# Kernel tuning notes

Hardware: AMD Instinct MI355X
Metric: run time of the kernel (lower is better)

## Reference

```python
import jax, jax.numpy as jnp
import numpy as np

B, N, M, C, H = 256, 4096, 64, 512, 4
IN, OUT = 64, 64
EPS = 1e-8

def setup_inputs():
    key = jax.random.key(0)
    ks = jax.random.split(key, 8)
    def w(k, shape, scale=0.05):
        return jax.random.normal(k, shape, dtype=jnp.float32) * scale
    return {
        "in_data": jax.random.normal(ks[0], (B, IN), dtype=jnp.float32),
        "memory": jax.random.normal(ks[1], (B, N, M), dtype=jnp.float32),
        "h0": jnp.zeros((B, C), jnp.float32),
        "c0": jnp.zeros((B, C), jnp.float32),
        "prev_weights": jnp.zeros((2 * H, B, N), jnp.float32),
        "prev_reads": jax.random.normal(ks[2], (H, B, M), dtype=jnp.float32),
        "W_ih": w(ks[3], (4 * C, IN + H * M)),
        "b_ih": jnp.zeros((4 * C,), jnp.float32),
        "W_hh": w(ks[4], (4 * C, C)),
        "b_hh": jnp.zeros((4 * C,), jnp.float32),
        "W_out": w(ks[5], (OUT, C + H * M)),
        "b_out": jnp.zeros((OUT,), jnp.float32),
        "W_addr": w(ks[6], (2 * H, M + 6, C)),
        "b_addr": jnp.zeros((2 * H, M + 6), jnp.float32),
        "W_ea": w(ks[7], (H, 2 * M, C)),
        "b_ea": jnp.zeros((H, 2 * M), jnp.float32),
    }


def reference(in_data, memory, h0, c0, prev_weights, prev_reads,
              W_ih, b_ih, W_hh, b_hh, W_out, b_out,
              W_addr, b_addr, W_ea, b_ea):
    # ---- controller: LSTMCell over [input, prev_reads...] ----
    x = jnp.concatenate([in_data] + [prev_reads[i] for i in range(H)], axis=-1)  # [B, IN+H*M]
    gates = x @ W_ih.T + b_ih + h0 @ W_hh.T + b_hh                               # [B, 4C]
    i_g, f_g, g_g, o_g = jnp.split(gates, 4, axis=-1)
    c = jax.nn.sigmoid(f_g) * c0 + jax.nn.sigmoid(i_g) * jnp.tanh(g_g)
    h = jax.nn.sigmoid(o_g) * jnp.tanh(c)

    # ---- heads: alternate read / write, sequential over memory ----
    mem = memory
    reads = []
    for hi in range(2 * H):
        p = c @ W_addr[hi].T + b_addr[hi]                     # [B, M+6]
        k = jnp.tanh(p[:, :M])                                # key
        beta = jax.nn.softplus(p[:, M:M + 1])                 # key strength
        gate = jax.nn.sigmoid(p[:, M + 1:M + 2])              # interpolation gate
        s = jax.nn.softmax(p[:, M + 2:M + 5], axis=-1)        # shift weights (3)
        gamma = 1.0 + jax.nn.softplus(p[:, M + 5:M + 6])      # sharpening
        # content addressing: cosine similarity against all memory rows
        dot = jnp.einsum('bnm,bm->bn', mem, k)                # [B, N]
        norms = jnp.linalg.norm(mem, axis=-1) * jnp.linalg.norm(k, axis=-1, keepdims=True)
        wc = jax.nn.softmax(beta * dot / (norms + EPS), axis=-1)
        # interpolation with previous weights
        wg = gate * wc + (1.0 - gate) * prev_weights[hi]
        # circular shift convolution (shifts -1, 0, +1)
        ws = (s[:, 0:1] * jnp.roll(wg, 1, axis=-1)
              + s[:, 1:2] * wg
              + s[:, 2:3] * jnp.roll(wg, -1, axis=-1))
        # sharpening
        wp = ws ** gamma
        w = wp / (jnp.sum(wp, axis=-1, keepdims=True) + EPS)
        if hi % 2 == 0:  # read head
            reads.append(jnp.einsum('bn,bnm->bm', w, mem))
        else:            # write head: erase then add
            ea = c @ W_ea[hi // 2].T + b_ea[hi // 2]          # [B, 2M]
            e = jax.nn.sigmoid(ea[:, :M])
            a = jnp.tanh(ea[:, M:])
            mem = mem * (1.0 - w[:, :, None] * e[:, None, :]) + w[:, :, None] * a[:, None, :]

    # ---- output layer over [h, reads...] ----
    state = jnp.concatenate([h] + reads, axis=-1)             # [B, C+H*M]
    return jax.nn.sigmoid(state @ W_out.T + b_out)            # [B, OUT]
```

## Files before the change

kernel.cpp:

```cpp
#include <hip/hip_runtime.h>
#include <hip/hip_fp16.h>
#include <math.h>

#define EPSF 1e-8f
#define NN 4096
#define BB 256
#define PH ((size_t)BB * NN)

__device__ __forceinline__ float sigf(float x) { return 1.0f / (1.0f + expf(-x)); }
__device__ __forceinline__ float softplusf(float x) { return x > 20.0f ? x : log1pf(expf(x)); }
__device__ __forceinline__ float dot4(float4 a, float4 b) {
  return a.x * b.x + a.y * b.y + a.z * b.z + a.w * b.w;
}
__device__ __forceinline__ unsigned short f2bf(float x) {
  unsigned int u = __float_as_uint(x);
  unsigned int r = (u + 0x7FFF + ((u >> 16) & 1)) >> 16;
  return (unsigned short)r;
}
__device__ __forceinline__ float bf2f(unsigned int lo16) {
  return __uint_as_float(lo16 << 16);
}

__device__ __forceinline__ float gather_x(const float* __restrict__ in_data,
                                          const float* __restrict__ prev_reads,
                                          const float* __restrict__ h0,
                                          int row, int k) {
  if (k < 64) return in_data[row * 64 + k];
  if (k < 320) { int i = (k - 64) >> 6, m = (k - 64) & 63; return prev_reads[((size_t)i * 256 + row) * 64 + m]; }
  return h0[row * 512 + (k - 320)];
}

__global__ __launch_bounds__(256) void gemm_gates_kernel(
    const float* __restrict__ in_data, const float* __restrict__ prev_reads,
    const float* __restrict__ h0, const float* __restrict__ W_ih,
    const float* __restrict__ W_hh, const float* __restrict__ b_ih,
    const float* __restrict__ b_hh, float* __restrict__ gates) {
  __shared__ float As[16][33];
  __shared__ float Ws[16][65];
  int tid = threadIdx.x, tx = tid & 15, ty = tid >> 4;
  int row0 = blockIdx.y * 32, col0 = blockIdx.x * 64;
  float acc[2][4] = {{0,0,0,0},{0,0,0,0}};
  for (int k0 = 0; k0 < 832; k0 += 16) {
    const float* Wp; int kw, KW;
    if (k0 < 320) { Wp = W_ih; kw = k0; KW = 320; }
    else          { Wp = W_hh; kw = k0 - 320; KW = 512; }
    for (int i = tid; i < 32 * 16; i += 256) {
      int rr = i >> 4, cc = i & 15;
      As[cc][rr] = gather_x(in_data, prev_reads, h0, row0 + rr, k0 + cc);
    }
    for (int i = tid; i < 64 * 16; i += 256) {
      int rr = i >> 4, cc = i & 15;
      Ws[cc][rr] = Wp[(size_t)(col0 + rr) * KW + kw + cc];
    }
    __syncthreads();
#pragma unroll
    for (int kk = 0; kk < 16; kk++) {
      float a0 = As[kk][ty * 2 + 0], a1 = As[kk][ty * 2 + 1];
      float w0 = Ws[kk][tx * 4 + 0], w1 = Ws[kk][tx * 4 + 1];
      float w2 = Ws[kk][tx * 4 + 2], w3 = Ws[kk][tx * 4 + 3];
      acc[0][0] += a0 * w0; acc[0][1] += a0 * w1; acc[0][2] += a0 * w2; acc[0][3] += a0 * w3;
      acc[1][0] += a1 * w0; acc[1][1] += a1 * w1; acc[1][2] += a1 * w2; acc[1][3] += a1 * w3;
    }
    __syncthreads();
  }
  for (int i = 0; i < 2; i++)
    for (int j = 0; j < 4; j++) {
      int cc = col0 + tx * 4 + j;
      gates[(size_t)(row0 + ty * 2 + i) * 2048 + cc] = acc[i][j] + b_ih[cc] + b_hh[cc];
    }
}

__global__ void lstm_elem_kernel(const float* __restrict__ gates,
                                 const float* __restrict__ c0,
                                 float* __restrict__ c, float* __restrict__ h) {
  int idx = blockIdx.x * 256 + threadIdx.x;
  if (idx >= 256 * 512) return;
  int b = idx >> 9, u = idx & 511;
  const float* g = gates + (size_t)b * 2048;
  float ig = sigf(g[u]), fg = sigf(g[512 + u]);
  float gg = tanhf(g[1024 + u]), og = sigf(g[1536 + u]);
  float cv = fg * c0[idx] + ig * gg;
  c[idx] = cv;
  h[idx] = og * tanhf(cv);
}

__global__ __launch_bounds__(256) void gemm_heads_kernel(
    const float* __restrict__ C, const float* __restrict__ W_addr,
    const float* __restrict__ W_ea, const float* __restrict__ b_addr,
    const float* __restrict__ b_ea, float* __restrict__ p_raw) {
  __shared__ float As[16][33];
  __shared__ float Ws[16][65];
  int tid = threadIdx.x, tx = tid & 15, ty = tid >> 4;
  int row0 = blockIdx.y * 32, col0 = blockIdx.x * 64;
  float acc[2][4] = {{0,0,0,0},{0,0,0,0}};
  for (int k0 = 0; k0 < 512; k0 += 16) {
    for (int i = tid; i < 32 * 16; i += 256) {
      int rr = i >> 4, cc = i & 15;
      As[cc][rr] = C[(size_t)(row0 + rr) * 512 + k0 + cc];
    }
    for (int i = tid; i < 64 * 16; i += 256) {
      int rr = i >> 4, cc = i & 15;
      int col = col0 + rr;
      float v = 0.f;
      if (col < 560) v = W_addr[(size_t)col * 512 + k0 + cc];
      else if (col < 1072) v = W_ea[(size_t)(col - 560) * 512 + k0 + cc];
      Ws[cc][rr] = v;
    }
    __syncthreads();
#pragma unroll
    for (int kk = 0; kk < 16; kk++) {
      float a0 = As[kk][ty * 2 + 0], a1 = As[kk][ty * 2 + 1];
      float w0 = Ws[kk][tx * 4 + 0], w1 = Ws[kk][tx * 4 + 1];
      float w2 = Ws[kk][tx * 4 + 2], w3 = Ws[kk][tx * 4 + 3];
      acc[0][0] += a0 * w0; acc[0][1] += a0 * w1; acc[0][2] += a0 * w2; acc[0][3] += a0 * w3;
      acc[1][0] += a1 * w0; acc[1][1] += a1 * w1; acc[1][2] += a1 * w2; acc[1][3] += a1 * w3;
    }
    __syncthreads();
  }
  for (int i = 0; i < 2; i++)
    for (int j = 0; j < 4; j++) {
      int col = col0 + tx * 4 + j;
      if (col < 1072) {
        float bias = col < 560 ? b_addr[col] : b_ea[col - 560];
        p_raw[(size_t)(row0 + ty * 2 + i) * 1072 + col] = acc[i][j] + bias;
      }
    }
}

__global__ void params_kernel(const float* __restrict__ p_raw,
    float* __restrict__ knorm, float* __restrict__ betav,
    float* __restrict__ gatev, float* __restrict__ sv,
    float* __restrict__ gammav, float* __restrict__ combo,
    float* __restrict__ scal) {
  int b = blockIdx.x, m = threadIdx.x;
  const float* p = p_raw + (size_t)b * 1072;
  float kv[7];
#pragma unroll
  for (int hi = 0; hi < 7; hi++) {
    float k = tanhf(p[hi * 70 + m]);
    kv[hi] = k;
    float s = k * k;
#pragma unroll
    for (int d = 1; d < 64; d <<= 1) s += __shfl_xor(s, d);
    if (m == 0) {
      int hb = hi * BB + b;
      knorm[hb] = sqrtf(s);
      betav[hb] = softplusf(p[hi * 70 + 64]);
      gatev[hb] = sigf(p[hi * 70 + 65]);
      float a0 = p[hi * 70 + 66], a1 = p[hi * 70 + 67], a2 = p[hi * 70 + 68];
      float mm = fmaxf(a0, fmaxf(a1, a2));
      float e0 = expf(a0 - mm), e1 = expf(a1 - mm), e2 = expf(a2 - mm);
      float es = e0 + e1 + e2;
      sv[hb * 3 + 0] = e0 / es; sv[hb * 3 + 1] = e1 / es; sv[hb * 3 + 2] = e2 / es;
      gammav[hb] = 1.0f + softplusf(p[hi * 70 + 69]);
    }
  }
  float e1 = sigf(p[560 + 0 * 128 + m]),  a1v = tanhf(p[560 + 0 * 128 + 64 + m]);
  float e3 = sigf(p[560 + 1 * 128 + m]),  a3v = tanhf(p[560 + 1 * 128 + 64 + m]);
  float e5 = sigf(p[560 + 2 * 128 + m]),  a5v = tanhf(p[560 + 2 * 128 + 64 + m]);
  size_t bm = (size_t)b * 64 + m;
  combo[0 * 16384 + bm] = kv[0];  combo[1 * 16384 + bm] = kv[1];
  combo[2 * 16384 + bm] = kv[2];  combo[3 * 16384 + bm] = e1 * kv[2];
  combo[4 * 16384 + bm] = kv[3];  combo[5 * 16384 + bm] = e1 * kv[3];
  combo[6 * 16384 + bm] = a1v;    combo[7 * 16384 + bm] = e1 * a1v;
  combo[8 * 16384 + bm] = e1;     combo[9 * 16384 + bm] = e1 * e1;
  combo[10 * 16384 + bm] = kv[4]; combo[11 * 16384 + bm] = kv[5];
  combo[12 * 16384 + bm] = kv[6]; combo[13 * 16384 + bm] = e5 * kv[6];
  combo[14 * 16384 + bm] = a5v;   combo[15 * 16384 + bm] = e5 * a5v;
  combo[16 * 16384 + bm] = e5;    combo[17 * 16384 + bm] = e5 * e5;
  combo[18 * 16384 + bm] = e3;    combo[19 * 16384 + bm] = a3v;
  float s0 = a1v * kv[2], s1 = a1v * kv[3], s2 = a1v * a1v, s3 = a5v * kv[6], s4 = a5v * a5v;
#pragma unroll
  for (int d = 1; d < 64; d <<= 1) {
    s0 += __shfl_xor(s0, d); s1 += __shfl_xor(s1, d); s2 += __shfl_xor(s2, d);
    s3 += __shfl_xor(s3, d); s4 += __shfl_xor(s4, d);
  }
  if (m == 0) {
    scal[b * 8 + 0] = s0; scal[b * 8 + 1] = s1; scal[b * 8 + 2] = s2;
    scal[b * 8 + 3] = s3; scal[b * 8 + 4] = s4;
  }
}

#define CL(j, q) (*(const float4*)(cb + (j) * 64 + (q) * 4))

__device__ void chain_dev(int tid, int b, int head,
    const __half* __restrict__ SC, const __half* __restrict__ Da,
    const __half* __restrict__ Dbc, const __half* __restrict__ S0p,
    const __half* __restrict__ T1p, const __half* __restrict__ T2p,
    const __half* w_h, int u_head, __half* w_out,
    float* wg, float* red,
    const float* __restrict__ knorm, const float* __restrict__ betav,
    const float* __restrict__ gatev, const float* __restrict__ sv,
    const float* __restrict__ gammav, const float* __restrict__ prev_w) {
  int lane = tid & 63, wv = tid >> 6;
  int hb = head * BB + b;
  float kn = knorm[hb], be = betav[hb], ga = gatev[hb], gm = gammav[hb];
  float s0 = sv[hb * 3 + 0], s1 = sv[hb * 3 + 1], s2 = sv[hb * 3 + 2];
  size_t bo = (size_t)b * NN;
  const float* pw = prev_w + (size_t)head * PH + bo;
  float sc[8];
  float mx = -1e30f;
#pragma unroll
  for (int i = 0; i < 8; i++) {
    int n = tid + i * 512;
    float scv;
    if (SC != nullptr) {
      scv = __half2float(SC[bo + n]);
    } else {
      float u = __half2float(w_h[u_head * NN + n]);
      float d = __half2float(Da[bo + n]) - u * __half2float(Dbc[bo + n]);
      float nn2 = __half2float(S0p[bo + n]) - 2.f * u * __half2float(T1p[bo + n])
                + u * u * __half2float(T2p[bo + n]);
      nn2 = fmaxf(nn2, 0.f);
      scv = be * d / (sqrtf(nn2) * kn + EPSF);
    }
    sc[i] = scv; mx = fmaxf(mx, scv);
  }
#pragma unroll
  for (int m = 1; m < 64; m <<= 1) mx = fmaxf(mx, __shfl_xor(mx, m));
  if (lane == 0) red[wv] = mx;
  __syncthreads();
  mx = red[0];
#pragma unroll
  for (int w = 1; w < 8; w++) mx = fmaxf(mx, red[w]);
  float sum = 0.f;
#pragma unroll
  for (int i = 0; i < 8; i++) { sc[i] = expf(sc[i] - mx); sum += sc[i]; }
#pragma unroll
  for (int m = 1; m < 64; m <<= 1) sum += __shfl_xor(sum, m);
  if (lane == 0) red[8 + wv] = sum;
  __syncthreads();
  sum = 0.f;
#pragma unroll
  for (int w = 0; w < 8; w++) sum += red[8 + w];
  float inv = 1.0f / sum;
#pragma unroll
  for (int i = 0; i < 8; i++) {
    int n = tid + i * 512;
    wg[n] = ga * (sc[i] * inv) + (1.f - ga) * pw[n];
  }
  __syncthreads();
  float wp[8];
  float sum2 = 0.f;
#pragma unroll
  for (int i = 0; i < 8; i++) {
    int n = tid + i * 512;
    float wsv = s0 * wg[(n + NN - 1) & (NN - 1)] + s1 * wg[n] + s2 * wg[(n + 1) & (NN - 1)];
    wp[i] = powf(wsv, gm);
    sum2 += wp[i];
  }
#pragma unroll
  for (int m = 1; m < 64; m <<= 1) sum2 += __shfl_xor(sum2, m);
  if (lane == 0) red[16 + wv] = sum2;
  __syncthreads();
  sum2 = 0.f;
#pragma unroll
  for (int w = 0; w < 8; w++) sum2 += red[16 + w];
  float invs = 1.0f / (sum2 + EPSF);
#pragma unroll
  for (int i = 0; i < 8; i++) {
    int n = tid + i * 512;
    w_out[n] = __float2half(wp[i] * invs);
  }
  __syncthreads();
}

__global__ __launch_bounds__(512, 2) void mega_kernel(
    const float* __restrict__ mem, const float* __restrict__ combo,
    const float* __restrict__ scal, const float* __restrict__ knorm,
    const float* __restrict__ betav, const float* __restrict__ gatev,
    const float* __restrict__ sv, const float* __restrict__ gammav,
    const float* __restrict__ prev_w, unsigned short* __restrict__ mem_bf,
    __half* __restrict__ P, float* __restrict__ reads) {
  extern __shared__ char smem[];
  __half* w_h   = (__half*)smem;
  float*  cb    = (float*)(smem + 57344);
  float*  scr   = (float*)(smem + 62464);
  char*   un    = smem + 84992;
  float4* tile32 = (float4*)un;
  uint4*  tileb  = (uint4*)un;
  float*  wg     = (float*)un;

  int b = blockIdx.x, tid = threadIdx.x;
  size_t bo = (size_t)b * NN;

  for (int i = tid; i < 1280; i += 512) {
    int j = i >> 6, m = i & 63;
    cb[i] = combo[(size_t)j * 16384 + b * 64 + m];
  }
  __syncthreads();

  {
    float kn0 = knorm[0 * BB + b], be0 = betav[0 * BB + b];
    float kn1 = knorm[1 * BB + b], be1 = betav[1 * BB + b];
    float cak2 = scal[b * 8 + 0], cak3 = scal[b * 8 + 1], caa1 = scal[b * 8 + 2];
    const float4* m4 = (const float4*)mem + bo * 16;
    ushort4* mb4 = (ushort4*)mem_bf + bo * 16;
    for (int c = 0; c < 16; c++) {
      int gbase = c * 4096;
#pragma unroll
      for (int i = 0; i < 8; i++) {
        int G = tid + i * 512;
        float4 v = m4[gbase + G];
        int r = G >> 4, q = G & 15;
        tile32[r * 16 + (q ^ (r & 15))] = v;
        ushort4 o;
        o.x = f2bf(v.x); o.y = f2bf(v.y); o.z = f2bf(v.z); o.w = f2bf(v.w);
        mb4[gbase + G] = o;
      }
      __syncthreads();
      int r = tid & 255, qb = (tid >> 8) * 8;
      float a[11];
#pragma unroll
      for (int k = 0; k < 11; k++) a[k] = 0.f;
#pragma unroll
      for (int j = 0; j < 8; j++) {
        int q = qb + j;
        float4 v = tile32[r * 16 + (q ^ (r & 15))];
        float4 sq = make_float4(v.x * v.x, v.y * v.y, v.z * v.z, v.w * v.w);
        a[0] += dot4(v, CL(0, q)); a[1] += dot4(v, CL(1, q));
        a[2] += dot4(v, CL(2, q)); a[3] += dot4(v, CL(3, q));
        a[4] += dot4(v, CL(4, q)); a[5] += dot4(v, CL(5, q));
        a[6] += dot4(v, CL(6, q)); a[7] += dot4(v, CL(7, q));
        a[8] += sq.x + sq.y + sq.z + sq.w;
        a[9] += dot4(sq, CL(8, q)); a[10] += dot4(sq, CL(9, q));
      }
#pragma unroll
      for (int k = 0; k < 11; k++) scr[tid * 11 + k] = a[k];
      __syncthreads();
      if (tid < 256) {
#pragma unroll
        for (int k = 0; k < 11; k++) a[k] = scr[tid * 11 + k] + scr[(tid + 256) * 11 + k];
        int n = c * 256 + tid;
        float rn = sqrtf(a[8]);
        P[0 * PH + bo + n] = __float2half(be0 * a[0] / (rn * kn0 + EPSF));
        P[1 * PH + bo + n] = __float2half(be1 * a[1] / (rn * kn1 + EPSF));
        P[2 * PH + bo + n] = __float2half(a[2]);
        P[3 * PH + bo + n] = __float2half(a[3] - cak2);
        P[4 * PH + bo + n] = __float2half(a[4]);
        P[5 * PH + bo + n] = __float2half(a[5] - cak3);
        P[6 * PH + bo + n] = __float2half(a[8]);
        P[7 * PH + bo + n] = __float2half(a[9] - a[6]);
        P[8 * PH + bo + n] = __float2half(a[10] - 2.f * a[7] + caa1);
      }
      __syncthreads();
    }
  }

  chain_dev(tid, b, 0, P + 0 * PH, nullptr, nullptr, nullptr, nullptr, nullptr,
            w_h, 0, w_h + 0 * NN, wg, scr, knorm, betav, gatev, sv, gammav, prev_w);
  chain_dev(tid, b, 1, P + 1 * PH, nullptr, nullptr, nullptr, nullptr, nullptr,
            w_h, 0, w_h + 1 * NN, wg, scr, knorm, betav, gatev, sv, gammav, prev_w);
  chain_dev(tid, b, 2, nullptr, P + 2 * PH, P + 3 * PH, P + 6 * PH, P + 7 * PH, P + 8 * PH,
            w_h, 1, w_h + 2 * NN, wg, scr, knorm, betav, gatev, sv, gammav, prev_w);
  chain_dev(tid, b, 3, nullptr, P + 4 * PH, P + 5 * PH, P + 6 * PH, P + 7 * PH, P + 8 * PH,
            w_h, 1, w_h + 3 * NN, wg, scr, knorm, betav, gatev, sv, gammav, prev_w);

  {
    float kn4 = knorm[4 * BB + b], be4 = betav[4 * BB + b];
    float kn5 = knorm[5 * BB + b], be5 = betav[5 * BB + b];
    float cak6 = scal[b * 8 + 3], caa5 = scal[b * 8 + 4];
    const uint4* mb16 = (const uint4*)mem_bf + bo * 8;
    for (int c = 0; c < 16; c++) {
      int gbase = c * 2048;
#pragma unroll
      for (int i = 0; i < 4; i++) {
        int G = tid + i * 512;
        uint4 u = mb16[gbase + G];
        int r = G >> 3, g = G & 7;
        tileb[r * 8 + (g ^ (r & 7))] = u;
      }
      __syncthreads();
      int r = tid & 255, gb2 = (tid >> 8) * 4;
      float u1 = __half2float(w_h[1 * NN + c * 256 + r]);
      float u3 = __half2float(w_h[3 * NN + c * 256 + r]);
      float t[9];
#pragma unroll
      for (int k = 0; k < 9; k++) t[k] = 0.f;
#pragma unroll
      for (int j = 0; j < 4; j++) {
        int g = gb2 + j;
        uint4 uv = tileb[r * 8 + (g ^ (r & 7))];
#pragma unroll
        for (int h = 0; h < 2; h++) {
          unsigned int pa = h ? uv.z : uv.x;
          unsigned int pb = h ? uv.w : uv.y;
          float4 v;
          v.x = bf2f(pa & 0xFFFFu); v.y = bf2f(pa >> 16);
          v.z = bf2f(pb & 0xFFFFu); v.w = bf2f(pb >> 16);
          int q = g * 2 + h;
          float4 e1v = CL(8, q), a1v = CL(6, q), e3v = CL(18, q), a3v = CL(19, q);
          float4 m1, m2;
          m1.x = v.x * (1.f - u1 * e1v.x) + u1 * a1v.x;
          m1.y = v.y * (1.f - u1 * e1v.y) + u1 * a1v.y;
          m1.z = v.z * (1.f - u1 * e1v.z) + u1 * a1v.z;
          m1.w = v.w * (1.f - u1 * e1v.w) + u1 * a1v.w;
          m2.x = m1.x * (1.f - u3 * e3v.x) + u3 * a3v.x;
          m2.y = m1.y * (1.f - u3 * e3v.y) + u3 * a3v.y;
          m2.z = m1.z * (1.f - u3 * e3v.z) + u3 * a3v.z;
          m2.w = m1.w * (1.f - u3 * e3v.w) + u3 * a3v.w;
          float4 sq = make_float4(m2.x * m2.x, m2.y * m2.y, m2.z * m2.z, m2.w * m2.w);
          t[0] += dot4(m2, CL(10, q)); t[1] += dot4(m2, CL(11, q));
          t[2] += dot4(m2, CL(12, q)); t[3] += dot4(m2, CL(13, q));
          t[4] += dot4(m2, CL(14, q)); t[5] += dot4(m2, CL(15, q));
          t[6] += sq.x + sq.y + sq.z + sq.w;
          t[7] += dot4(sq, CL(16, q)); t[8] += dot4(sq, CL(17, q));
        }
      }
#pragma unroll
      for (int k = 0; k < 9; k++) scr[tid * 9 + k] = t[k];
      __syncthreads();
      if (tid < 256) {
#pragma unroll
        for (int k = 0; k < 9; k++) t[k] = scr[tid * 9 + k] + scr[(tid + 256) * 9 + k];
        int n = c * 256 + tid;
        float rn = sqrtf(t[6]);
        P[0 * PH + bo + n] = __float2half(be4 * t[0] / (rn * kn4 + EPSF));
        P[1 * PH + bo + n] = __float2half(be5 * t[1] / (rn * kn5 + EPSF));
        P[2 * PH + bo + n] = __float2half(t[2]);
        P[3 * PH + bo + n] = __float2half(t[3] - cak6);
        P[4 * PH + bo + n] = __float2half(t[6]);
        P[5 * PH + bo + n] = __float2half(t[7] - t[4]);
        P[6 * PH + bo + n] = __float2half(t[8] - 2.f * t[5] + caa5);
      }
      __syncthreads();
    }
  }

  chain_dev(tid, b, 4, P + 0 * PH, nullptr, nullptr, nullptr, nullptr, nullptr,
            w_h, 0, w_h + 4 * NN, wg, scr, knorm, betav, gatev, sv, gammav, prev_w);
  chain_dev(tid, b, 5, P + 1 * PH, nullptr, nullptr, nullptr, nullptr, nullptr,
            w_h, 0, w_h + 5 * NN, wg, scr, knorm, betav, gatev, sv, gammav, prev_w);
  chain_dev(tid, b, 6, nullptr, P + 2 * PH, P + 3 * PH, P + 4 * PH, P + 5 * PH, P + 6 * PH,
            w_h, 5, w_h + 6 * NN, wg, scr, knorm, betav, gatev, sv, gammav, prev_w);

  {
    int wv = tid >> 6, lane = tid & 63, q = lane & 15, rl = lane >> 4;
    float4 e1v = CL(8, q), a1v = CL(6, q), e3v = CL(18, q), a3v = CL(19, q);
    float4 e5v = CL(16, q), a5v = CL(14, q);
    const ushort4* mbr = (const ushort4*)mem_bf + bo * 16;
    float A[4][4];
#pragma unroll
    for (int j = 0; j < 4; j++)
#pragma unroll
      for (int cmp = 0; cmp < 4; cmp++) A[j][cmp] = 0.f;
#pragma unroll 4
    for (int t = 0; t < 128; t++) {
      int n = t * 32 + wv * 4 + rl;
      ushort4 uv = mbr[(size_t)n * 16 + q];
      float vx = bf2f(uv.x), vy = bf2f(uv.y), vz = bf2f(uv.z), vw = bf2f(uv.w);
      float w0v = __half2float(w_h[0 * NN + n]);
      float u1  = __half2float(w_h[1 * NN + n]);
      float w2v = __half2float(w_h[2 * NN + n]);
      float u3  = __half2float(w_h[3 * NN + n]);
      float w4v = __half2float(w_h[4 * NN + n]);
      float u5  = __half2float(w_h[5 * NN + n]);
      float w6v = __half2float(w_h[6 * NN + n]);
      A[0][0] += w0v * vx; A[0][1] += w0v * vy; A[0][2] += w0v * vz; A[0][3] += w0v * vw;
      float m1x = vx * (1.f - u1 * e1v.x) + u1 * a1v.x;
      float m1y = vy * (1.f - u1 * e1v.y) + u1 * a1v.y;
      float m1z = vz * (1.f - u1 * e1v.z) + u1 * a1v.z;
      float m1w = vw * (1.f - u1 * e1v.w) + u1 * a1v.w;
      A[1][0] += w2v * m1x; A[1][1] += w2v * m1y; A[1][2] += w2v * m1z; A[1][3] += w2v * m1w;
      float m2x = m1x * (1.f - u3 * e3v.x) + u3 * a3v.x;
      float m2y = m1y * (1.f - u3 * e3v.y) + u3 * a3v.y;
      float m2z = m1z * (1.f - u3 * e3v.z) + u3 * a3v.z;
      float m2w = m1w * (1.f - u3 * e3v.w) + u3 * a3v.w;
      A[2][0] += w4v * m2x; A[2][1] += w4v * m2y; A[2][2] += w4v * m2z; A[2][3] += w4v * m2w;
      float m3x = m2x * (1.f - u5 * e5v.x) + u5 * a5v.x;
      float m3y = m2y * (1.f - u5 * e5v.y) + u5 * a5v.y;
      float m3z = m2z * (1.f - u5 * e5v.z) + u5 * a5v.z;
      float m3w = m2w * (1.f - u5 * e5v.w) + u5 * a5v.w;
      A[3][0] += w6v * m3x; A[3][1] += w6v * m3y; A[3][2] += w6v * m3z; A[3][3] += w6v * m3w;
    }
#pragma unroll
    for (int j = 0; j < 4; j++)
#pragma unroll
      for (int cmp = 0; cmp < 4; cmp++) {
        float x = A[j][cmp];
        x += __shfl_xor(x, 16);
        x += __shfl_xor(x, 32);
        A[j][cmp] = x;
      }
    float* sred = scr;
    if (rl == 0)
#pragma unroll
      for (int j = 0; j < 4; j++)
#pragma unroll
        for (int cmp = 0; cmp < 4; cmp++)
          sred[((j * 8 + wv) * 16 + q) * 4 + cmp] = A[j][cmp];
    __syncthreads();
    if (tid < 256) {
      int j = tid >> 6, qq = (tid >> 2) & 15, cc = tid & 3;
      float s = 0.f;
#pragma unroll
      for (int w = 0; w < 8; w++) s += sred[((j * 8 + w) * 16 + qq) * 4 + cc];
      reads[(size_t)j * 16384 + b * 64 + qq * 4 + cc] = s;
    }
  }
}

__global__ __launch_bounds__(256) void gemm_out_kernel(
    const float* __restrict__ h, const float* __restrict__ reads,
    const float* __restrict__ W_out, const float* __restrict__ b_out,
    float* __restrict__ out) {
  __shared__ float As[16][33];
  __shared__ float Ws[16][65];
  int tid = threadIdx.x, tx = tid & 15, ty = tid >> 4;
  int row0 = blockIdx.y * 32;
  float acc[2][4] = {{0,0,0,0},{0,0,0,0}};
  for (int k0 = 0; k0 < 768; k0 += 16) {
    for (int i = tid; i < 32 * 16; i += 256) {
      int rr = i >> 4, cc = i & 15;
      int row = row0 + rr, k = k0 + cc;
      float v;
      if (k < 512) v = h[row * 512 + k];
      else { int slot = (k - 512) >> 6, m = (k - 512) & 63; v = reads[((size_t)slot * 256 + row) * 64 + m]; }
      As[cc][rr] = v;
    }
    for (int i = tid; i < 64 * 16; i += 256) {
      int rr = i >> 4, cc = i & 15;
      Ws[cc][rr] = W_out[(size_t)rr * 768 + k0 + cc];
    }
    __syncthreads();
#pragma unroll
    for (int kk = 0; kk < 16; kk++) {
      float a0 = As[kk][ty * 2 + 0], a1 = As[kk][ty * 2 + 1];
      float w0 = Ws[kk][tx * 4 + 0], w1 = Ws[kk][tx * 4 + 1];
      float w2 = Ws[kk][tx * 4 + 2], w3 = Ws[kk][tx * 4 + 3];
      acc[0][0] += a0 * w0; acc[0][1] += a0 * w1; acc[0][2] += a0 * w2; acc[0][3] += a0 * w3;
      acc[1][0] += a1 * w0; acc[1][1] += a1 * w1; acc[1][2] += a1 * w2; acc[1][3] += a1 * w3;
    }
    __syncthreads();
  }
  for (int i = 0; i < 2; i++)
    for (int j = 0; j < 4; j++) {
      int cc = tx * 4 + j;
      out[(size_t)(row0 + ty * 2 + i) * 64 + cc] = sigf(acc[i][j] + b_out[cc]);
    }
}

extern "C" void kernel_launch(void* const* d_in, const int* in_sizes, int n_in,
                              void* d_out, int out_size, void* d_ws, size_t ws_size,
                              hipStream_t stream) {
  const float* in_data = (const float*)d_in[0];
  const float* memory  = (const float*)d_in[1];
  const float* h0      = (const float*)d_in[2];
  const float* c0      = (const float*)d_in[3];
  const float* prev_w  = (const float*)d_in[4];
  const float* prev_r  = (const float*)d_in[5];
  const float* W_ih    = (const float*)d_in[6];
  const float* b_ih    = (const float*)d_in[7];
  const float* W_hh    = (const float*)d_in[8];
  const float* b_hh    = (const float*)d_in[9];
  const float* W_out   = (const float*)d_in[10];
  const float* b_out   = (const float*)d_in[11];
  const float* W_addr  = (const float*)d_in[12];
  const float* b_addr  = (const float*)d_in[13];
  const float* W_ea    = (const float*)d_in[14];
  const float* b_ea    = (const float*)d_in[15];
  float* out = (float*)d_out;
  (void)in_sizes; (void)n_in; (void)out_size; (void)ws_size;

  float* ws = (float*)d_ws;
  size_t off = 0;
  auto alloc = [&](size_t n) { float* p = ws + off; off += (n + 63) & ~(size_t)63; return p; };
  float* gates  = alloc(256 * 2048);
  float* cbuf   = alloc(256 * 512);
  float* hbuf   = alloc(256 * 512);
  float* p_raw  = alloc(256 * 1072);
  float* knorm  = alloc(8 * 256);
  float* betav  = alloc(8 * 256);
  float* gatev  = alloc(8 * 256);
  float* sv     = alloc(8 * 256 * 3);
  float* gammav = alloc(8 * 256);
  float* combo  = alloc(20 * 16384);
  float* scal   = alloc(256 * 8);
  __half* P     = (__half*)alloc(9 * PH / 2);
  float* reads  = alloc(4 * 16384);
  unsigned short* mem_bf = (unsigned short*)alloc(33554432);

  static bool attr_set = false;
  if (!attr_set) {
    hipFuncSetAttribute((const void*)mega_kernel,
                        hipFuncAttributeMaxDynamicSharedMemorySize, 150528);
    attr_set = true;
  }

  gemm_gates_kernel<<<dim3(32, 8), 256, 0, stream>>>(in_data, prev_r, h0, W_ih, W_hh, b_ih, b_hh, gates);
  lstm_elem_kernel<<<(256 * 512 + 255) / 256, 256, 0, stream>>>(gates, c0, cbuf, hbuf);
  gemm_heads_kernel<<<dim3(17, 8), 256, 0, stream>>>(cbuf, W_addr, W_ea, b_addr, b_ea, p_raw);
  params_kernel<<<256, 64, 0, stream>>>(p_raw, knorm, betav, gatev, sv, gammav, combo, scal);
  mega_kernel<<<256, 512, 150528, stream>>>(memory, combo, scal, knorm, betav, gatev,
                                            sv, gammav, prev_w, mem_bf, P, reads);
  gemm_out_kernel<<<dim3(1, 8), 256, 0, stream>>>(hbuf, reads, W_out, b_out, out);
}
```

Measured before the change: 903.2 us.

## Split per-batch mega kernel into multi-phase kernels with wider grids

Replaces the single mega kernel (256 blocks, one per batch row, with heavy shared memory) with separate phase kernels. The memory-scan phases use 16 blocks per batch row, the head chains run in parallel across independent heads, and the final read pass is split over 8 chunks with atomicAdd into a zeroed reads buffer. Head weights move from shared memory into a global w_g buffer. This is meant to raise occupancy and parallelism beyond 256 blocks, at the cost of extra launches, global round trips for the weights, and atomics.

```diff
diff --git a/kernel.cpp b/kernel.cpp
--- a/kernel.cpp
+++ b/kernel.cpp
@@ -183,21 +183,78 @@
 
 #define CL(j, q) (*(const float4*)(cb + (j) * 64 + (q) * 4))
 
-__device__ void chain_dev(int tid, int b, int head,
-    const __half* __restrict__ SC, const __half* __restrict__ Da,
-    const __half* __restrict__ Dbc, const __half* __restrict__ S0p,
-    const __half* __restrict__ T1p, const __half* __restrict__ T2p,
-    const __half* w_h, int u_head, __half* w_out,
-    float* wg, float* red,
+__global__ __launch_bounds__(256) void phase1_kernel(
+    const float* __restrict__ mem, const float* __restrict__ combo,
+    const float* __restrict__ scal, const float* __restrict__ knorm,
+    const float* __restrict__ betav, unsigned short* __restrict__ mem_bf,
+    __half* __restrict__ P) {
+  __shared__ float cb[640];
+  int b = blockIdx.y, tid = threadIdx.x;
+  for (int i = tid; i < 640; i += 256)
+    cb[i] = combo[(size_t)(i >> 6) * 16384 + b * 64 + (i & 63)];
+  __syncthreads();
+  float kn0 = knorm[b], be0 = betav[b];
+  float kn1 = knorm[BB + b], be1 = betav[BB + b];
+  float cak2 = scal[b * 8 + 0], cak3 = scal[b * 8 + 1], caa1 = scal[b * 8 + 2];
+  int n = blockIdx.x * 256 + tid;
+  size_t bo = (size_t)b * NN;
+  const float4* rp = (const float4*)mem + (bo + n) * 16;
+  ushort4* op = (ushort4*)mem_bf + (bo + n) * 16;
+  float a[11];
+#pragma unroll
+  for (int k = 0; k < 11; k++) a[k] = 0.f;
+#pragma unroll
+  for (int q = 0; q < 16; q++) {
+    float4 v = rp[q];
+    ushort4 o;
+    o.x = f2bf(v.x); o.y = f2bf(v.y); o.z = f2bf(v.z); o.w = f2bf(v.w);
+    op[q] = o;
+    float4 sq = make_float4(v.x * v.x, v.y * v.y, v.z * v.z, v.w * v.w);
+    a[0] += dot4(v, CL(0, q)); a[1] += dot4(v, CL(1, q));
+    a[2] += dot4(v, CL(2, q)); a[3] += dot4(v, CL(3, q));
+    a[4] += dot4(v, CL(4, q)); a[5] += dot4(v, CL(5, q));
+    a[6] += dot4(v, CL(6, q)); a[7] += dot4(v, CL(7, q));
+    a[8] += sq.x + sq.y + sq.z + sq.w;
+    a[9] += dot4(sq, CL(8, q)); a[10] += dot4(sq, CL(9, q));
+  }
+  float rn = sqrtf(a[8]);
+  P[0 * PH + bo + n] = __float2half(be0 * a[0] / (rn * kn0 + EPSF));
+  P[1 * PH + bo + n] = __float2half(be1 * a[1] / (rn * kn1 + EPSF));
+  P[2 * PH + bo + n] = __float2half(a[2]);
+  P[3 * PH + bo + n] = __float2half(a[3] - cak2);
+  P[4 * PH + bo + n] = __float2half(a[4]);
+  P[5 * PH + bo + n] = __float2half(a[5] - cak3);
+  P[6 * PH + bo + n] = __float2half(a[8]);
+  P[7 * PH + bo + n] = __float2half(a[9] - a[6]);
+  P[8 * PH + bo + n] = __float2half(a[10] - 2.f * a[7] + caa1);
+}
+
+__global__ __launch_bounds__(512) void chain_kernel(
+    const __half* __restrict__ P, __half* __restrict__ w_g,
     const float* __restrict__ knorm, const float* __restrict__ betav,
     const float* __restrict__ gatev, const float* __restrict__ sv,
-    const float* __restrict__ gammav, const float* __restrict__ prev_w) {
+    const float* __restrict__ gammav, const float* __restrict__ prev_w,
+    int group) {
+  __shared__ float wg[NN];
+  __shared__ float red[24];
+  int b = blockIdx.x, hy = blockIdx.y, tid = threadIdx.x;
   int lane = tid & 63, wv = tid >> 6;
+  int head, u_head = 0;
+  const __half *SC = nullptr, *Da = nullptr, *Dbc = nullptr;
+  const __half *S0p = nullptr, *T1p = nullptr, *T2p = nullptr;
+  if (group == 0)      { head = hy;     SC = P + (size_t)hy * PH; }
+  else if (group == 1) { head = 2 + hy; Da = P + (size_t)(2 + 2 * hy) * PH; Dbc = P + (size_t)(3 + 2 * hy) * PH;
+                         S0p = P + 6 * PH; T1p = P + 7 * PH; T2p = P + 8 * PH; u_head = 1; }
+  else if (group == 2) { head = 4 + hy; SC = P + (size_t)hy * PH; }
+  else                 { head = 6;      Da = P + 2 * PH; Dbc = P + 3 * PH;
+                         S0p = P + 4 * PH; T1p = P + 5 * PH; T2p = P + 6 * PH; u_head = 5; }
   int hb = head * BB + b;
   float kn = knorm[hb], be = betav[hb], ga = gatev[hb], gm = gammav[hb];
   float s0 = sv[hb * 3 + 0], s1 = sv[hb * 3 + 1], s2 = sv[hb * 3 + 2];
   size_t bo = (size_t)b * NN;
   const float* pw = prev_w + (size_t)head * PH + bo;
+  const __half* ug = w_g + ((size_t)u_head * BB + b) * NN;
+  __half* wout = w_g + ((size_t)head * BB + b) * NN;
   float sc[8];
   float mx = -1e30f;
 #pragma unroll
@@ -207,7 +264,7 @@
     if (SC != nullptr) {
       scv = __half2float(SC[bo + n]);
     } else {
-      float u = __half2float(w_h[u_head * NN + n]);
+      float u = __half2float(ug[n]);
       float d = __half2float(Da[bo + n]) - u * __half2float(Dbc[bo + n]);
       float nn2 = __half2float(S0p[bo + n]) - 2.f * u * __half2float(T1p[bo + n])
                 + u * u * __half2float(T2p[bo + n]);
@@ -260,243 +317,147 @@
 #pragma unroll
   for (int i = 0; i < 8; i++) {
     int n = tid + i * 512;
-    w_out[n] = __float2half(wp[i] * invs);
-  }
-  __syncthreads();
-}
-
-__global__ __launch_bounds__(512, 2) void mega_kernel(
-    const float* __restrict__ mem, const float* __restrict__ combo,
+    wout[n] = __float2half(wp[i] * invs);
+  }
+}
+
+__global__ __launch_bounds__(256) void phase2_kernel(
+    const unsigned short* __restrict__ mem_bf, const float* __restrict__ combo,
     const float* __restrict__ scal, const float* __restrict__ knorm,
-    const float* __restrict__ betav, const float* __restrict__ gatev,
-    const float* __restrict__ sv, const float* __restrict__ gammav,
-    const float* __restrict__ prev_w, unsigned short* __restrict__ mem_bf,
-    __half* __restrict__ P, float* __restrict__ reads) {
-  extern __shared__ char smem[];
-  __half* w_h   = (__half*)smem;
-  float*  cb    = (float*)(smem + 57344);
-  float*  scr   = (float*)(smem + 62464);
-  char*   un    = smem + 84992;
-  float4* tile32 = (float4*)un;
-  uint4*  tileb  = (uint4*)un;
-  float*  wg     = (float*)un;
-
-  int b = blockIdx.x, tid = threadIdx.x;
+    const float* __restrict__ betav, const __half* __restrict__ w_g,
+    __half* __restrict__ P) {
+  __shared__ float cb[1280];
+  int b = blockIdx.y, tid = threadIdx.x;
+  for (int i = tid; i < 1280; i += 256)
+    cb[i] = combo[(size_t)(i >> 6) * 16384 + b * 64 + (i & 63)];
+  __syncthreads();
+  float kn4 = knorm[4 * BB + b], be4 = betav[4 * BB + b];
+  float kn5 = knorm[5 * BB + b], be5 = betav[5 * BB + b];
+  float cak6 = scal[b * 8 + 3], caa5 = scal[b * 8 + 4];
+  int n = blockIdx.x * 256 + tid;
   size_t bo = (size_t)b * NN;
-
-  for (int i = tid; i < 1280; i += 512) {
-    int j = i >> 6, m = i & 63;
-    cb[i] = combo[(size_t)j * 16384 + b * 64 + m];
-  }
-  __syncthreads();
-
-  {
-    float kn0 = knorm[0 * BB + b], be0 = betav[0 * BB + b];
-    float kn1 = knorm[1 * BB + b], be1 = betav[1 * BB + b];
-    float cak2 = scal[b * 8 + 0], cak3 = scal[b * 8 + 1], caa1 = scal[b * 8 + 2];
-    const float4* m4 = (const float4*)mem + bo * 16;
-    ushort4* mb4 = (ushort4*)mem_bf + bo * 16;
-    for (int c = 0; c < 16; c++) {
-      int gbase = c * 4096;
-#pragma unroll
-      for (int i = 0; i < 8; i++) {
-        int G = tid + i * 512;
-        float4 v = m4[gbase + G];
-        int r = G >> 4, q = G & 15;
-        tile32[r * 16 + (q ^ (r & 15))] = v;
-        ushort4 o;
-        o.x = f2bf(v.x); o.y = f2bf(v.y); o.z = f2bf(v.z); o.w = f2bf(v.w);
-        mb4[gbase + G] = o;
-      }
-      __syncthreads();
-      int r = tid & 255, qb = (tid >> 8) * 8;
-      float a[11];
-#pragma unroll
-      for (int k = 0; k < 11; k++) a[k] = 0.f;
-#pragma unroll
-      for (int j = 0; j < 8; j++) {
-        int q = qb + j;
-        float4 v = tile32[r * 16 + (q ^ (r & 15))];
-        float4 sq = make_float4(v.x * v.x, v.y * v.y, v.z * v.z, v.w * v.w);
-        a[0] += dot4(v, CL(0, q)); a[1] += dot4(v, CL(1, q));
-        a[2] += dot4(v, CL(2, q)); a[3] += dot4(v, CL(3, q));
-        a[4] += dot4(v, CL(4, q)); a[5] += dot4(v, CL(5, q));
-        a[6] += dot4(v, CL(6, q)); a[7] += dot4(v, CL(7, q));
-        a[8] += sq.x + sq.y + sq.z + sq.w;
-        a[9] += dot4(sq, CL(8, q)); a[10] += dot4(sq, CL(9, q));
-      }
-#pragma unroll
-      for (int k = 0; k < 11; k++) scr[tid * 11 + k] = a[k];
-      __syncthreads();
-      if (tid < 256) {
-#pragma unroll
-        for (int k = 0; k < 11; k++) a[k] = scr[tid * 11 + k] + scr[(tid + 256) * 11 + k];
-        int n = c * 256 + tid;
-        float rn = sqrtf(a[8]);
-        P[0 * PH + bo + n] = __float2half(be0 * a[0] / (rn * kn0 + EPSF));
-        P[1 * PH + bo + n] = __float2half(be1 * a[1] / (rn * kn1 + EPSF));
-        P[2 * PH + bo + n] = __float2half(a[2]);
-        P[3 * PH + bo + n] = __float2half(a[3] - cak2);
-        P[4 * PH + bo + n] = __float2half(a[4]);
-        P[5 * PH + bo + n] = __float2half(a[5] - cak3);
-        P[6 * PH + bo + n] = __float2half(a[8]);
-        P[7 * PH + bo + n] = __float2half(a[9] - a[6]);
-        P[8 * PH + bo + n] = __float2half(a[10] - 2.f * a[7] + caa1);
-      }
-      __syncthreads();
-    }
-  }
-
-  chain_dev(tid, b, 0, P + 0 * PH, nullptr, nullptr, nullptr, nullptr, nullptr,
-            w_h, 0, w_h + 0 * NN, wg, scr, knorm, betav, gatev, sv, gammav, prev_w);
-  chain_dev(tid, b, 1, P + 1 * PH, nullptr, nullptr, nullptr, nullptr, nullptr,
-            w_h, 0, w_h + 1 * NN, wg, scr, knorm, betav, gatev, sv, gammav, prev_w);
-  chain_dev(tid, b, 2, nullptr, P + 2 * PH, P + 3 * PH, P + 6 * PH, P + 7 * PH, P + 8 * PH,
-            w_h, 1, w_h + 2 * NN, wg, scr, knorm, betav, gatev, sv, gammav, prev_w);
-  chain_dev(tid, b, 3, nullptr, P + 4 * PH, P + 5 * PH, P + 6 * PH, P + 7 * PH, P + 8 * PH,
-            w_h, 1, w_h + 3 * NN, wg, scr, knorm, betav, gatev, sv, gammav, prev_w);
-
-  {
-    float kn4 = knorm[4 * BB + b], be4 = betav[4 * BB + b];
-    float kn5 = knorm[5 * BB + b], be5 = betav[5 * BB + b];
-    float cak6 = scal[b * 8 + 3], caa5 = scal[b * 8 + 4];
-    const uint4* mb16 = (const uint4*)mem_bf + bo * 8;
-    for (int c = 0; c < 16; c++) {
-      int gbase = c * 2048;
-#pragma unroll
-      for (int i = 0; i < 4; i++) {
-        int G = tid + i * 512;
-        uint4 u = mb16[gbase + G];
-        int r = G >> 3, g = G & 7;
-        tileb[r * 8 + (g ^ (r & 7))] = u;
-      }
-      __syncthreads();
-      int r = tid & 255, gb2 = (tid >> 8) * 4;
-      float u1 = __half2float(w_h[1 * NN + c * 256 + r]);
-      float u3 = __half2float(w_h[3 * NN + c * 256 + r]);
-      float t[9];
-#pragma unroll
-      for (int k = 0; k < 9; k++) t[k] = 0.f;
-#pragma unroll
-      for (int j = 0; j < 4; j++) {
-        int g = gb2 + j;
-        uint4 uv = tileb[r * 8 + (g ^ (r & 7))];
-#pragma unroll
-        for (int h = 0; h < 2; h++) {
-          unsigned int pa = h ? uv.z : uv.x;
-          unsigned int pb = h ? uv.w : uv.y;
-          float4 v;
-          v.x = bf2f(pa & 0xFFFFu); v.y = bf2f(pa >> 16);
-          v.z = bf2f(pb & 0xFFFFu); v.w = bf2f(pb >> 16);
-          int q = g * 2 + h;
-          float4 e1v = CL(8, q), a1v = CL(6, q), e3v = CL(18, q), a3v = CL(19, q);
-          float4 m1, m2;
-          m1.x = v.x * (1.f - u1 * e1v.x) + u1 * a1v.x;
-          m1.y = v.y * (1.f - u1 * e1v.y) + u1 * a1v.y;
-          m1.z = v.z * (1.f - u1 * e1v.z) + u1 * a1v.z;
-          m1.w = v.w * (1.f - u1 * e1v.w) + u1 * a1v.w;
-          m2.x = m1.x * (1.f - u3 * e3v.x) + u3 * a3v.x;
-          m2.y = m1.y * (1.f - u3 * e3v.y) + u3 * a3v.y;
-          m2.z = m1.z * (1.f - u3 * e3v.z) + u3 * a3v.z;
-          m2.w = m1.w * (1.f - u3 * e3v.w) + u3 * a3v.w;
-          float4 sq = make_float4(m2.x * m2.x, m2.y * m2.y, m2.z * m2.z, m2.w * m2.w);
-          t[0] += dot4(m2, CL(10, q)); t[1] += dot4(m2, CL(11, q));
-          t[2] += dot4(m2, CL(12, q)); t[3] += dot4(m2, CL(13, q));
-          t[4] += dot4(m2, CL(14, q)); t[5] += dot4(m2, CL(15, q));
-          t[6] += sq.x + sq.y + sq.z + sq.w;
-          t[7] += dot4(sq, CL(16, q)); t[8] += dot4(sq, CL(17, q));
-        }
-      }
-#pragma unroll
-      for (int k = 0; k < 9; k++) scr[tid * 9 + k] = t[k];
-      __syncthreads();
-      if (tid < 256) {
-#pragma unroll
-        for (int k = 0; k < 9; k++) t[k] = scr[tid * 9 + k] + scr[(tid + 256) * 9 + k];
-        int n = c * 256 + tid;
-        float rn = sqrtf(t[6]);
-        P[0 * PH + bo + n] = __float2half(be4 * t[0] / (rn * kn4 + EPSF));
-        P[1 * PH + bo + n] = __float2half(be5 * t[1] / (rn * kn5 + EPSF));
-        P[2 * PH + bo + n] = __float2half(t[2]);
-        P[3 * PH + bo + n] = __float2half(t[3] - cak6);
-        P[4 * PH + bo + n] = __float2half(t[6]);
-        P[5 * PH + bo + n] = __float2half(t[7] - t[4]);
-        P[6 * PH + bo + n] = __float2half(t[8] - 2.f * t[5] + caa5);
-      }
-      __syncthreads();
-    }
-  }
-
-  chain_dev(tid, b, 4, P + 0 * PH, nullptr, nullptr, nullptr, nullptr, nullptr,
-            w_h, 0, w_h + 4 * NN, wg, scr, knorm, betav, gatev, sv, gammav, prev_w);
-  chain_dev(tid, b, 5, P + 1 * PH, nullptr, nullptr, nullptr, nullptr, nullptr,
-            w_h, 0, w_h + 5 * NN, wg, scr, knorm, betav, gatev, sv, gammav, prev_w);
-  chain_dev(tid, b, 6, nullptr, P + 2 * PH, P + 3 * PH, P + 4 * PH, P + 5 * PH, P + 6 * PH,
-            w_h, 5, w_h + 6 * NN, wg, scr, knorm, betav, gatev, sv, gammav, prev_w);
-
-  {
-    int wv = tid >> 6, lane = tid & 63, q = lane & 15, rl = lane >> 4;
-    float4 e1v = CL(8, q), a1v = CL(6, q), e3v = CL(18, q), a3v = CL(19, q);
-    float4 e5v = CL(16, q), a5v = CL(14, q);
-    const ushort4* mbr = (const ushort4*)mem_bf + bo * 16;
-    float A[4][4];
+  const uint4* mb = (const uint4*)mem_bf + (bo + n) * 8;
+  float u1 = __half2float(w_g[((size_t)1 * BB + b) * NN + n]);
+  float u3 = __half2float(w_g[((size_t)3 * BB + b) * NN + n]);
+  float t[9];
+#pragma unroll
+  for (int k = 0; k < 9; k++) t[k] = 0.f;
+#pragma unroll
+  for (int g = 0; g < 8; g++) {
+    uint4 uv = mb[g];
+#pragma unroll
+    for (int h = 0; h < 2; h++) {
+      unsigned int pa = h ? uv.z : uv.x;
+      unsigned int pb = h ? uv.w : uv.y;
+      float4 v;
+      v.x = bf2f(pa & 0xFFFFu); v.y = bf2f(pa >> 16);
+      v.z = bf2f(pb & 0xFFFFu); v.w = bf2f(pb >> 16);
+      int q = g * 2 + h;
+      float4 e1v = CL(8, q), a1v = CL(6, q), e3v = CL(18, q), a3v = CL(19, q);
+      float4 m1, m2;
+      m1.x = v.x * (1.f - u1 * e1v.x) + u1 * a1v.x;
+      m1.y = v.y * (1.f - u1 * e1v.y) + u1 * a1v.y;
+      m1.z = v.z * (1.f - u1 * e1v.z) + u1 * a1v.z;
+      m1.w = v.w * (1.f - u1 * e1v.w) + u1 * a1v.w;
+      m2.x = m1.x * (1.f - u3 * e3v.x) + u3 * a3v.x;
+      m2.y = m1.y * (1.f - u3 * e3v.y) + u3 * a3v.y;
+      m2.z = m1.z * (1.f - u3 * e3v.z) + u3 * a3v.z;
+      m2.w = m1.w * (1.f - u3 * e3v.w) + u3 * a3v.w;
+      float4 sq = make_float4(m2.x * m2.x, m2.y * m2.y, m2.z * m2.z, m2.w * m2.w);
+      t[0] += dot4(m2, CL(10, q)); t[1] += dot4(m2, CL(11, q));
+      t[2] += dot4(m2, CL(12, q)); t[3] += dot4(m2, CL(13, q));
+      t[4] += dot4(m2, CL(14, q)); t[5] += dot4(m2, CL(15, q));
+      t[6] += sq.x + sq.y + sq.z + sq.w;
+      t[7] += dot4(sq, CL(16, q)); t[8] += dot4(sq, CL(17, q));
+    }
+  }
+  float rn = sqrtf(t[6]);
+  P[0 * PH + bo + n] = __float2half(be4 * t[0] / (rn * kn4 + EPSF));
+  P[1 * PH + bo + n] = __float2half(be5 * t[1] / (rn * kn5 + EPSF));
+  P[2 * PH + bo + n] = __float2half(t[2]);
+  P[3 * PH + bo + n] = __float2half(t[3] - cak6);
+  P[4 * PH + bo + n] = __float2half(t[6]);
+  P[5 * PH + bo + n] = __float2half(t[7] - t[4]);
+  P[6 * PH + bo + n] = __float2half(t[8] - 2.f * t[5] + caa5);
+}
+
+__global__ __launch_bounds__(256) void phase3_kernel(
+    const unsigned short* __restrict__ mem_bf, const float* __restrict__ combo,
+    const __half* __restrict__ w_g, float* __restrict__ reads) {
+  __shared__ float cb[1280];
+  __shared__ __half ws[7 * 512];
+  __shared__ float sred[4 * 4 * 16 * 4];
+  int b = blockIdx.y, chunk = blockIdx.x, tid = threadIdx.x;
+  for (int i = tid; i < 1280; i += 256)
+    cb[i] = combo[(size_t)(i >> 6) * 16384 + b * 64 + (i & 63)];
+  int nbase = chunk * 512;
+  for (int i = tid; i < 7 * 512; i += 256) {
+    int hh = i >> 9, nn = i & 511;
+    ws[i] = w_g[((size_t)hh * BB + b) * NN + nbase + nn];
+  }
+  __syncthreads();
+  int wv = tid >> 6, lane = tid & 63, q = lane & 15, rl = lane >> 4;
+  float4 e1v = CL(8, q), a1v = CL(6, q), e3v = CL(18, q), a3v = CL(19, q);
+  float4 e5v = CL(16, q), a5v = CL(14, q);
+  size_t bo = (size_t)b * NN;
+  const ushort4* mbr = (const ushort4*)mem_bf + bo * 16;
+  float A[4][4];
+#pragma unroll
+  for (int j = 0; j < 4; j++)
+#pragma unroll
+    for (int cmp = 0; cmp < 4; cmp++) A[j][cmp] = 0.f;
+#pragma unroll 4
+  for (int t = 0; t < 32; t++) {
+    int nl = t * 16 + wv * 4 + rl;
+    int n = nbase + nl;
+    ushort4 uv = mbr[(size_t)n * 16 + q];
+    float vx = bf2f(uv.x), vy = bf2f(uv.y), vz = bf2f(uv.z), vw = bf2f(uv.w);
+    float w0v = __half2float(ws[0 * 512 + nl]);
+    float u1  = __half2float(ws[1 * 512 + nl]);
+    float w2v = __half2float(ws[2 * 512 + nl]);
+    float u3  = __half2float(ws[3 * 512 + nl]);
+    float w4v = __half2float(ws[4 * 512 + nl]);
+    float u5  = __half2float(ws[5 * 512 + nl]);
+    float w6v = __half2float(ws[6 * 512 + nl]);
+    A[0][0] += w0v * vx; A[0][1] += w0v * vy; A[0][2] += w0v * vz; A[0][3] += w0v * vw;
+    float m1x = vx * (1.f - u1 * e1v.x) + u1 * a1v.x;
+    float m1y = vy * (1.f - u1 * e1v.y) + u1 * a1v.y;
+    float m1z = vz * (1.f - u1 * e1v.z) + u1 * a1v.z;
+    float m1w = vw * (1.f - u1 * e1v.w) + u1 * a1v.w;
+    A[1][0] += w2v * m1x; A[1][1] += w2v * m1y; A[1][2] += w2v * m1z; A[1][3] += w2v * m1w;
+    float m2x = m1x * (1.f - u3 * e3v.x) + u3 * a3v.x;
+    float m2y = m1y * (1.f - u3 * e3v.y) + u3 * a3v.y;
+    float m2z = m1z * (1.f - u3 * e3v.z) + u3 * a3v.z;
+    float m2w = m1w * (1.f - u3 * e3v.w) + u3 * a3v.w;
+    A[2][0] += w4v * m2x; A[2][1] += w4v * m2y; A[2][2] += w4v * m2z; A[2][3] += w4v * m2w;
+    float m3x = m2x * (1.f - u5 * e5v.x) + u5 * a5v.x;
+    float m3y = m2y * (1.f - u5 * e5v.y) + u5 * a5v.y;
+    float m3z = m2z * (1.f - u5 * e5v.z) + u5 * a5v.z;
+    float m3w = m2w * (1.f - u5 * e5v.w) + u5 * a5v.w;
+    A[3][0] += w6v * m3x; A[3][1] += w6v * m3y; A[3][2] += w6v * m3z; A[3][3] += w6v * m3w;
+  }
+#pragma unroll
+  for (int j = 0; j < 4; j++)
+#pragma unroll
+    for (int cmp = 0; cmp < 4; cmp++) {
+      float x = A[j][cmp];
+      x += __shfl_xor(x, 16);
+      x += __shfl_xor(x, 32);
+      A[j][cmp] = x;
+    }
+  if (rl == 0)
 #pragma unroll
     for (int j = 0; j < 4; j++)
 #pragma unroll
-      for (int cmp = 0; cmp < 4; cmp++) A[j][cmp] = 0.f;
-#pragma unroll 4
-    for (int t = 0; t < 128; t++) {
-      int n = t * 32 + wv * 4 + rl;
-      ushort4 uv = mbr[(size_t)n * 16 + q];
-      float vx = bf2f(uv.x), vy = bf2f(uv.y), vz = bf2f(uv.z), vw = bf2f(uv.w);
-      float w0v = __half2float(w_h[0 * NN + n]);
-      float u1  = __half2float(w_h[1 * NN + n]);
-      float w2v = __half2float(w_h[2 * NN + n]);
-      float u3  = __half2float(w_h[3 * NN + n]);
-      float w4v = __half2float(w_h[4 * NN + n]);
-      float u5  = __half2float(w_h[5 * NN + n]);
-      float w6v = __half2float(w_h[6 * NN + n]);
-      A[0][0] += w0v * vx; A[0][1] += w0v * vy; A[0][2] += w0v * vz; A[0][3] += w0v * vw;
-      float m1x = vx * (1.f - u1 * e1v.x) + u1 * a1v.x;
-      float m1y = vy * (1.f - u1 * e1v.y) + u1 * a1v.y;
-      float m1z = vz * (1.f - u1 * e1v.z) + u1 * a1v.z;
-      float m1w = vw * (1.f - u1 * e1v.w) + u1 * a1v.w;
-      A[1][0] += w2v * m1x; A[1][1] += w2v * m1y; A[1][2] += w2v * m1z; A[1][3] += w2v * m1w;
-      float m2x = m1x * (1.f - u3 * e3v.x) + u3 * a3v.x;
-      float m2y = m1y * (1.f - u3 * e3v.y) + u3 * a3v.y;
-      float m2z = m1z * (1.f - u3 * e3v.z) + u3 * a3v.z;
-      float m2w = m1w * (1.f - u3 * e3v.w) + u3 * a3v.w;
-      A[2][0] += w4v * m2x; A[2][1] += w4v * m2y; A[2][2] += w4v * m2z; A[2][3] += w4v * m2w;
-      float m3x = m2x * (1.f - u5 * e5v.x) + u5 * a5v.x;
-      float m3y = m2y * (1.f - u5 * e5v.y) + u5 * a5v.y;
-      float m3z = m2z * (1.f - u5 * e5v.z) + u5 * a5v.z;
-      float m3w = m2w * (1.f - u5 * e5v.w) + u5 * a5v.w;
-      A[3][0] += w6v * m3x; A[3][1] += w6v * m3y; A[3][2] += w6v * m3z; A[3][3] += w6v * m3w;
-    }
-#pragma unroll
-    for (int j = 0; j < 4; j++)
-#pragma unroll
-      for (int cmp = 0; cmp < 4; cmp++) {
-        float x = A[j][cmp];
-        x += __shfl_xor(x, 16);
-        x += __shfl_xor(x, 32);
-        A[j][cmp] = x;
-      }
-    float* sred = scr;
-    if (rl == 0)
-#pragma unroll
-      for (int j = 0; j < 4; j++)
-#pragma unroll
-        for (int cmp = 0; cmp < 4; cmp++)
-          sred[((j * 8 + wv) * 16 + q) * 4 + cmp] = A[j][cmp];
-    __syncthreads();
-    if (tid < 256) {
-      int j = tid >> 6, qq = (tid >> 2) & 15, cc = tid & 3;
-      float s = 0.f;
-#pragma unroll
-      for (int w = 0; w < 8; w++) s += sred[((j * 8 + w) * 16 + qq) * 4 + cc];
-      reads[(size_t)j * 16384 + b * 64 + qq * 4 + cc] = s;
-    }
+      for (int cmp = 0; cmp < 4; cmp++)
+        sred[((j * 4 + wv) * 16 + q) * 4 + cmp] = A[j][cmp];
+  __syncthreads();
+  if (tid < 256) {
+    int j = tid >> 6, qq = (tid >> 2) & 15, cc = tid & 3;
+    float s = 0.f;
+#pragma unroll
+    for (int w = 0; w < 4; w++) s += sred[((j * 4 + w) * 16 + qq) * 4 + cc];
+    atomicAdd(&reads[(size_t)j * 16384 + b * 64 + qq * 4 + cc], s);
   }
 }
 
@@ -579,19 +540,21 @@
   __half* P     = (__half*)alloc(9 * PH / 2);
   float* reads  = alloc(4 * 16384);
   unsigned short* mem_bf = (unsigned short*)alloc(33554432);
-
-  static bool attr_set = false;
-  if (!attr_set) {
-    hipFuncSetAttribute((const void*)mega_kernel,
-                        hipFuncAttributeMaxDynamicSharedMemorySize, 150528);
-    attr_set = true;
-  }
+  __half* w_g   = (__half*)alloc(7 * BB * NN / 2);
 
   gemm_gates_kernel<<<dim3(32, 8), 256, 0, stream>>>(in_data, prev_r, h0, W_ih, W_hh, b_ih, b_hh, gates);
   lstm_elem_kernel<<<(256 * 512 + 255) / 256, 256, 0, stream>>>(gates, c0, cbuf, hbuf);
   gemm_heads_kernel<<<dim3(17, 8), 256, 0, stream>>>(cbuf, W_addr, W_ea, b_addr, b_ea, p_raw);
   params_kernel<<<256, 64, 0, stream>>>(p_raw, knorm, betav, gatev, sv, gammav, combo, scal);
-  mega_kernel<<<256, 512, 150528, stream>>>(memory, combo, scal, knorm, betav, gatev,
-                                            sv, gammav, prev_w, mem_bf, P, reads);
+  hipMemsetAsync(reads, 0, 4 * 16384 * sizeof(float), stream);
+
+  phase1_kernel<<<dim3(16, 256), 256, 0, stream>>>(memory, combo, scal, knorm, betav, mem_bf, P);
+  chain_kernel<<<dim3(256, 2), 512, 0, stream>>>(P, w_g, knorm, betav, gatev, sv, gammav, prev_w, 0);
+  chain_kernel<<<dim3(256, 2), 512, 0, stream>>>(P, w_g, knorm, betav, gatev, sv, gammav, prev_w, 1);
+  phase2_kernel<<<dim3(16, 256), 256, 0, stream>>>(mem_bf, combo, scal, knorm, betav, w_g, P);
+  chain_kernel<<<dim3(256, 2), 512, 0, stream>>>(P, w_g, knorm, betav, gatev, sv, gammav, prev_w, 2);
+  chain_kernel<<<dim3(256, 1), 512, 0, stream>>>(P, w_g, knorm, betav, gatev, sv, gammav, prev_w, 3);
+  phase3_kernel<<<dim3(8, 256), 256, 0, stream>>>(mem_bf, combo, w_g, reads);
+
   gemm_out_kernel<<<dim3(1, 8), 256, 0, stream>>>(hbuf, reads, W_out, b_out, out);
 }
```

Result: slower. 968.0 us (+7.2%).
